# Kernel optimization log

Hardware: AMD Instinct MI355X
Metric: run time of the kernel (lower is better)

The kernel has to match this reference:

```python
import jax, jax.numpy as jnp
import numpy as np

B, SQ, QD = 8, 4096, 1280
SCTX, CD = 93, 2048
HEADS, DIM_HEAD = 20, 64
INNER = HEADS * DIM_HEAD  # 1280


def setup_inputs() -> dict:
    key = jax.random.key(0)
    ks = jax.random.split(key, 10)
    inp = {
        'x': jax.random.normal(ks[0], (B, SQ, QD), dtype=jnp.float32),
        'context': jax.random.normal(ks[1], (B, SCTX, CD), dtype=jnp.float32),
        'scale': jax.random.uniform(ks[2], (), dtype=jnp.float32),
        'num_img_token': 16,
        # learned parameters (PyTorch nn.Linear weight layout: [out, in])
        'Wq': jax.random.normal(ks[3], (INNER, QD), dtype=jnp.float32) * 0.02,
        'Wk': jax.random.normal(ks[4], (INNER, CD), dtype=jnp.float32) * 0.02,
        'Wv': jax.random.normal(ks[5], (INNER, CD), dtype=jnp.float32) * 0.02,
        'Wk_ip': jax.random.normal(ks[6], (INNER, CD), dtype=jnp.float32) * 0.02,
        'Wv_ip': jax.random.normal(ks[7], (INNER, CD), dtype=jnp.float32) * 0.02,
        'Wout': jax.random.normal(ks[8], (QD, INNER), dtype=jnp.float32) * 0.02,
        'b_out': jax.random.normal(ks[9], (QD,), dtype=jnp.float32) * 0.02,
    }
    return inp


def _heads(t):
    # [b, s, inner] -> [b, h, s, d]
    b, s, _ = t.shape
    return t.reshape(b, s, HEADS, DIM_HEAD).transpose(0, 2, 1, 3)


def _attn(q, k, v):
    # q: [b,h,sq,d], k/v: [b,h,skv,d]
    sm_scale = 1.0 / jnp.sqrt(jnp.asarray(DIM_HEAD, q.dtype))
    logits = jnp.einsum('bhqd,bhkd->bhqk', q, k) * sm_scale
    probs = jax.nn.softmax(logits, axis=-1)
    return jnp.einsum('bhqk,bhkd->bhqd', probs, v)


def reference(x, context, scale, num_img_token, Wq, Wk, Wv, Wk_ip, Wv_ip, Wout, b_out):
    eos = context.shape[1] - num_img_token
    txt_ctx = context[:, :eos, :]
    img_ctx = context[:, eos:, :]

    q = _heads(jnp.einsum('bsc,ic->bsi', x, Wq))
    k = _heads(jnp.einsum('bsc,ic->bsi', txt_ctx, Wk))
    v = _heads(jnp.einsum('bsc,ic->bsi', txt_ctx, Wv))
    k_i = _heads(jnp.einsum('bsc,ic->bsi', img_ctx, Wk_ip))
    v_i = _heads(jnp.einsum('bsc,ic->bsi', img_ctx, Wv_ip))

    txt_out = _attn(q, k, v)            # [b,h,sq,d]
    img_out = _attn(q, k_i, v_i)        # [b,h,sq,d]
    out = txt_out + scale * img_out

    out = out.transpose(0, 2, 1, 3).reshape(x.shape[0], x.shape[1], INNER)
    return jnp.einsum('bsi,oi->bso', out, Wout) + b_out
```

## Files before the change

kernel.cpp:

```cpp
#include <hip/hip_runtime.h>
#include <stdint.h>
#include <stddef.h>

typedef __attribute__((ext_vector_type(8))) short bf16x8;
typedef __attribute__((ext_vector_type(4))) short bf16x4;
typedef __attribute__((ext_vector_type(4))) float f32x4;

typedef const __attribute__((address_space(1))) uint32_t gas_u32;
typedef __attribute__((address_space(3))) uint32_t las_u32;

__device__ __forceinline__ short f2bf(float f) {
  union { float f; uint32_t u; } c; c.f = f;
  uint32_t u = c.u;
  u += 0x7fffu + ((u >> 16) & 1u);
  return (short)(u >> 16);
}

__global__ void k_cvt(const float* __restrict__ src, short* __restrict__ dst, int n) {
  int i = (blockIdx.x * 256 + threadIdx.x) * 4;
  if (i + 4 <= n) {
    float4 v = *(const float4*)(src + i);
    bf16x4 o = { f2bf(v.x), f2bf(v.y), f2bf(v.z), f2bf(v.w) };
    *(bf16x4*)(dst + i) = o;
  } else {
    for (; i < n; ++i) dst[i] = f2bf(src[i]);
  }
}

__global__ void k_cvt_ctx(const float* __restrict__ ctx, short* __restrict__ dst,
                          int rpb, int row0) {
  long total = 8L * rpb * 2048;
  long i = ((long)blockIdx.x * 256 + threadIdx.x) * 4;
  if (i >= total) return;
  int c = (int)(i & 2047);
  long rs = i >> 11;
  int b = (int)(rs / rpb);
  int s = (int)(rs - (long)b * rpb);
  const float* sp = ctx + ((long)(b * 93 + row0 + s) * 2048 + c);
  float4 v = *(const float4*)sp;
  bf16x4 o = { f2bf(v.x), f2bf(v.y), f2bf(v.z), f2bf(v.w) };
  *(bf16x4*)(dst + i) = o;
}

template <int MODE>
__global__ __launch_bounds__(256)
void k_gemm(const short* __restrict__ A, const short* __restrict__ Bm,
            void* __restrict__ out, const float* __restrict__ bias,
            int Mreal, int N, int K, int SPB) {
  __shared__ __align__(16) short As[128 * 32];
  __shared__ __align__(16) short Bs[128 * 32];
  const int t = threadIdx.x;
  const int lane = t & 63, wave = t >> 6;
  const int wm = (wave >> 1) * 64, wn = (wave & 1) * 64;
  const int m0 = blockIdx.y * 128, n0 = blockIdx.x * 128;
  const int q4 = lane >> 4, r16 = lane & 15;

  f32x4 zero = {0.f, 0.f, 0.f, 0.f};
  f32x4 acc[4][4];
#pragma unroll
  for (int i = 0; i < 4; ++i)
#pragma unroll
    for (int j = 0; j < 4; ++j) acc[i][j] = zero;

  const int p0 = t, p1 = t + 256;
  const int ar0 = p0 >> 2, ac0 = (((p0 & 3) ^ ((ar0 >> 1) & 3))) * 8;
  const int ar1 = p1 >> 2, ac1 = (((p1 & 3) ^ ((ar1 >> 1) & 3))) * 8;
  int gm0 = m0 + ar0; if (gm0 >= Mreal) gm0 = Mreal - 1;
  int gm1 = m0 + ar1; if (gm1 >= Mreal) gm1 = Mreal - 1;
  const short* ga0 = A + (size_t)gm0 * K + ac0;
  const short* ga1 = A + (size_t)gm1 * K + ac1;
  const short* gb0 = Bm + (size_t)(n0 + ar0) * K + ac0;
  const short* gb1 = Bm + (size_t)(n0 + ar1) * K + ac1;

  const int swz = (q4 ^ ((r16 >> 1) & 3)) * 8;

  for (int k0 = 0; k0 < K; k0 += 32) {
    __builtin_amdgcn_global_load_lds((gas_u32*)(ga0 + k0), (las_u32*)(As + p0 * 8), 16, 0, 0);
    __builtin_amdgcn_global_load_lds((gas_u32*)(ga1 + k0), (las_u32*)(As + p1 * 8), 16, 0, 0);
    __builtin_amdgcn_global_load_lds((gas_u32*)(gb0 + k0), (las_u32*)(Bs + p0 * 8), 16, 0, 0);
    __builtin_amdgcn_global_load_lds((gas_u32*)(gb1 + k0), (las_u32*)(Bs + p1 * 8), 16, 0, 0);
    __syncthreads();

    bf16x8 af[4], bf[4];
#pragma unroll
    for (int i = 0; i < 4; ++i)
      af[i] = *(const bf16x8*)(As + (wm + i * 16 + r16) * 32 + swz);
#pragma unroll
    for (int j = 0; j < 4; ++j)
      bf[j] = *(const bf16x8*)(Bs + (wn + j * 16 + r16) * 32 + swz);
#pragma unroll
    for (int i = 0; i < 4; ++i)
#pragma unroll
      for (int j = 0; j < 4; ++j)
        acc[i][j] = __builtin_amdgcn_mfma_f32_16x16x32_bf16(af[i], bf[j], acc[i][j], 0, 0, 0);
    __syncthreads();
  }

  if (MODE == 0) {
    short* O = (short*)out;
#pragma unroll
    for (int i = 0; i < 4; ++i) {
#pragma unroll
      for (int rr = 0; rr < 4; ++rr) {
        int m = m0 + wm + i * 16 + q4 * 4 + rr;
        if (m < Mreal) {
          int bb, ss;
          if (SPB == 4096) { bb = m >> 12; ss = m & 4095; }
          else             { bb = m / SPB; ss = m - bb * SPB; }
#pragma unroll
          for (int j = 0; j < 4; ++j) {
            int n = n0 + wn + j * 16 + r16;
            int h = n >> 6, d = n & 63;
            int grp = (h >= 20) ? 1 : 0;
            int hl = h - grp * 20;
            O[(((size_t)(grp * 160 + bb * 20 + hl)) * SPB + ss) * 64 + d] = f2bf(acc[i][j][rr]);
          }
        }
      }
    }
  } else {
    float* O = (float*)out;
#pragma unroll
    for (int i = 0; i < 4; ++i) {
#pragma unroll
      for (int rr = 0; rr < 4; ++rr) {
        int m = m0 + wm + i * 16 + q4 * 4 + rr;
        if (m < Mreal) {
#pragma unroll
          for (int j = 0; j < 4; ++j) {
            int n = n0 + wn + j * 16 + r16;
            O[(size_t)m * N + n] = acc[i][j][rr] + bias[n];
          }
        }
      }
    }
  }
}

__global__ __launch_bounds__(256)
void k_attn(const short* __restrict__ qb, const short* __restrict__ kb,
            const short* __restrict__ vb, const short* __restrict__ kib,
            const short* __restrict__ vib, const float* __restrict__ scale_p,
            short* __restrict__ out) {
  constexpr int KS = 72;
  constexpr int PS = 104;
  __shared__ __align__(16) short Ks[96 * KS];
  __shared__ __align__(16) short Vt[64 * PS];
  __shared__ __align__(16) short Pp[4][16 * PS];
  const int t = threadIdx.x, lane = t & 63, wave = t >> 6;
  const int q4 = lane >> 4, r16 = lane & 15;
  const int b = blockIdx.z, h = blockIdx.y, qt = blockIdx.x;
  const int bh = b * 20 + h;
  const short* kt = kb + (size_t)bh * 77 * 64;
  const short* vt = vb + (size_t)bh * 77 * 64;
  const short* ki = kib + (size_t)bh * 16 * 64;
  const short* vi = vib + (size_t)bh * 16 * 64;

  for (int c = t; c < 96 * 8; c += 256) {
    int row = c >> 3, o = (c & 7) * 8;
    uint4 val = {0u, 0u, 0u, 0u};
    if (row < 77)       val = *(const uint4*)(kt + row * 64 + o);
    else if (row >= 80) val = *(const uint4*)(ki + (row - 80) * 64 + o);
    *(uint4*)(Ks + row * KS + o) = val;
  }
  for (int i = t; i < 96 * 64; i += 256) {
    int key = i >> 6, d = i & 63;
    short v = 0;
    if (key < 77)       v = vt[key * 64 + d];
    else if (key >= 80) v = vi[(key - 80) * 64 + d];
    Vt[d * PS + key] = v;
  }
  __syncthreads();

  const int s0 = qt * 64 + wave * 16;
  const short* qp = qb + ((size_t)bh * 4096 + s0) * 64;
  bf16x8 qf[2];
#pragma unroll
  for (int kc = 0; kc < 2; ++kc)
    qf[kc] = *(const bf16x8*)(qp + r16 * 64 + kc * 32 + q4 * 8);

  f32x4 zero = {0.f, 0.f, 0.f, 0.f};
  f32x4 lg[6];
#pragma unroll
  for (int nt = 0; nt < 6; ++nt) {
    lg[nt] = zero;
#pragma unroll
    for (int kc = 0; kc < 2; ++kc) {
      bf16x8 kf = *(const bf16x8*)(Ks + (nt * 16 + r16) * KS + kc * 32 + q4 * 8);
      lg[nt] = __builtin_amdgcn_mfma_f32_16x16x32_bf16(qf[kc], kf, lg[nt], 0, 0, 0);
    }
  }

  const float sm = 0.125f;
  const float scl = scale_p[0];
#pragma unroll
  for (int nt = 0; nt < 6; ++nt)
#pragma unroll
    for (int rr = 0; rr < 4; ++rr) lg[nt][rr] *= sm;
  if (r16 >= 13) {
#pragma unroll
    for (int rr = 0; rr < 4; ++rr) lg[4][rr] = -1e30f;
  }

#pragma unroll
  for (int rr = 0; rr < 4; ++rr) {
    float mx = -1e30f;
#pragma unroll
    for (int nt = 0; nt < 5; ++nt) mx = fmaxf(mx, lg[nt][rr]);
#pragma unroll
    for (int o = 1; o < 16; o <<= 1) mx = fmaxf(mx, __shfl_xor(mx, o, 64));
    float s = 0.f;
#pragma unroll
    for (int nt = 0; nt < 5; ++nt) {
      float p = __expf(lg[nt][rr] - mx);
      lg[nt][rr] = p; s += p;
    }
#pragma unroll
    for (int o = 1; o < 16; o <<= 1) s += __shfl_xor(s, o, 64);
    float inv = 1.f / s;
#pragma unroll
    for (int nt = 0; nt < 5; ++nt) lg[nt][rr] *= inv;

    float mi = lg[5][rr];
#pragma unroll
    for (int o = 1; o < 16; o <<= 1) mi = fmaxf(mi, __shfl_xor(mi, o, 64));
    float pi = __expf(lg[5][rr] - mi);
    float si = pi;
#pragma unroll
    for (int o = 1; o < 16; o <<= 1) si += __shfl_xor(si, o, 64);
    lg[5][rr] = pi * (scl / si);
  }

  short* pw = &Pp[wave][0];
#pragma unroll
  for (int nt = 0; nt < 6; ++nt)
#pragma unroll
    for (int rr = 0; rr < 4; ++rr)
      pw[(q4 * 4 + rr) * PS + nt * 16 + r16] = f2bf(lg[nt][rr]);

  f32x4 oc[4];
#pragma unroll
  for (int dt = 0; dt < 4; ++dt) {
    oc[dt] = zero;
#pragma unroll
    for (int kc = 0; kc < 3; ++kc) {
      bf16x8 pf = *(const bf16x8*)(pw + r16 * PS + kc * 32 + q4 * 8);
      bf16x8 vf = *(const bf16x8*)(Vt + (dt * 16 + r16) * PS + kc * 32 + q4 * 8);
      oc[dt] = __builtin_amdgcn_mfma_f32_16x16x32_bf16(pf, vf, oc[dt], 0, 0, 0);
    }
  }

#pragma unroll
  for (int dt = 0; dt < 4; ++dt)
#pragma unroll
    for (int rr = 0; rr < 4; ++rr) {
      int m = s0 + q4 * 4 + rr;
      int d = dt * 16 + r16;
      out[((size_t)b * 4096 + m) * 1280 + h * 64 + d] = f2bf(oc[dt][rr]);
    }
}

extern "C" void kernel_launch(void* const* d_in, const int* in_sizes, int n_in,
                              void* d_out, int out_size, void* d_ws, size_t ws_size,
                              hipStream_t stream) {
  const float* x    = (const float*)d_in[0];
  const float* ctx  = (const float*)d_in[1];
  const float* scal = (const float*)d_in[2];
  const float* Wq   = (const float*)d_in[4];
  const float* Wk   = (const float*)d_in[5];
  const float* Wv   = (const float*)d_in[6];
  const float* Wkip = (const float*)d_in[7];
  const float* Wvip = (const float*)d_in[8];
  const float* Wout = (const float*)d_in[9];
  const float* bout = (const float*)d_in[10];
  float* out = (float*)d_out;

  char* ws = (char*)d_ws;
  size_t off = 0;
  auto alloc = [&](size_t elems) -> short* {
    short* p = (short*)(ws + off);
    off += (elems * 2 + 255) & ~(size_t)255;
    return p;
  };
  short* xb    = alloc(32768UL * 1280);
  short* txtb  = alloc(616UL * 2048);
  short* imgb  = alloc(128UL * 2048);
  short* Wqb   = alloc(1280UL * 1280);
  short* Wkvb  = alloc(2UL * 1280 * 2048);
  short* Wkvip = alloc(2UL * 1280 * 2048);
  short* Woutb = alloc(1280UL * 1280);
  short* qb    = alloc(32768UL * 1280);
  short* kb    = alloc(2UL * 160 * 77 * 64);
  short* kib   = alloc(2UL * 160 * 16 * 64);
  short* vb    = kb  + 160UL * 77 * 64;
  short* vib   = kib + 160UL * 16 * 64;
  short* attnb = xb;

  auto cvt = [&](const float* s, short* d, long n) {
    int blocks = (int)((n / 4 + 255) / 256);
    k_cvt<<<blocks, 256, 0, stream>>>(s, d, (int)n);
  };
  cvt(x, xb, 32768L * 1280);
  cvt(Wq, Wqb, 1280L * 1280);
  cvt(Wk,   Wkvb,                 1280L * 2048);
  cvt(Wv,   Wkvb + 1280L * 2048,  1280L * 2048);
  cvt(Wkip, Wkvip,                1280L * 2048);
  cvt(Wvip, Wkvip + 1280L * 2048, 1280L * 2048);
  cvt(Wout, Woutb, 1280L * 1280);
  {
    long n1 = 8L * 77 * 2048;
    k_cvt_ctx<<<(int)((n1 / 4 + 255) / 256), 256, 0, stream>>>(ctx, txtb, 77, 0);
    long n2 = 8L * 16 * 2048;
    k_cvt_ctx<<<(int)((n2 / 4 + 255) / 256), 256, 0, stream>>>(ctx, imgb, 16, 77);
  }

  { dim3 g(10, 256); k_gemm<0><<<g, 256, 0, stream>>>(xb, Wqb, qb, nullptr, 32768, 1280, 1280, 4096); }
  { dim3 g(20, 5);
    k_gemm<0><<<g, 256, 0, stream>>>(txtb, Wkvb, kb, nullptr, 616, 2560, 2048, 77); }
  { dim3 g(20, 1);
    k_gemm<0><<<g, 256, 0, stream>>>(imgb, Wkvip, kib, nullptr, 128, 2560, 2048, 16); }
  { dim3 g(64, 20, 8);
    k_attn<<<g, 256, 0, stream>>>(qb, kb, vb, kib, vib, scal, attnb); }
  { dim3 g(10, 256);
    k_gemm<1><<<g, 256, 0, stream>>>(attnb, Woutb, out, bout, 32768, 1280, 1280, 1); }
}
```

Baseline: 884.0 us.

## Use 256x256 multi-stage pipelined GEMM, batch conversions and KV projections

Replaces the 128x128 single-buffered GEMM with a 256x256-tile, 512-thread kernel. It keeps four LDS stages with explicit vmcnt waits so global loads overlap MFMA work, raises MFMA priority with setprio, and remaps workgroups in XCD-aware order. The seven fp32-to-bf16 conversion launches are merged into one multi-segment kernel, and the text and image K/V projections share a single launch. The cost is 128KB of LDS per block and more registers per thread, which may reduce occupancy; the small K/V GEMMs also waste more work in padded tiles.

```diff
diff --git a/kernel.cpp b/kernel.cpp
--- a/kernel.cpp
+++ b/kernel.cpp
@@ -16,15 +16,21 @@
   return (short)(u >> 16);
 }
 
-__global__ void k_cvt(const float* __restrict__ src, short* __restrict__ dst, int n) {
-  int i = (blockIdx.x * 256 + threadIdx.x) * 4;
-  if (i + 4 <= n) {
-    float4 v = *(const float4*)(src + i);
-    bf16x4 o = { f2bf(v.x), f2bf(v.y), f2bf(v.z), f2bf(v.w) };
-    *(bf16x4*)(dst + i) = o;
-  } else {
-    for (; i < n; ++i) dst[i] = f2bf(src[i]);
-  }
+struct CvtArgs {
+  const float* s[7];
+  short* d[7];
+  long cum[8];
+};
+
+__global__ void k_cvt_multi(CvtArgs a) {
+  long i = ((long)blockIdx.x * 256 + threadIdx.x) * 4;
+  if (i >= a.cum[7]) return;
+  int g = 0;
+  while (i >= a.cum[g + 1]) ++g;
+  long o = i - a.cum[g];
+  float4 v = *(const float4*)(a.s[g] + o);
+  bf16x4 ov = { f2bf(v.x), f2bf(v.y), f2bf(v.z), f2bf(v.w) };
+  *(bf16x4*)(a.d[g] + o) = ov;
 }
 
 __global__ void k_cvt_ctx(const float* __restrict__ ctx, short* __restrict__ dst,
@@ -43,89 +49,132 @@
 }
 
 template <int MODE>
-__global__ __launch_bounds__(256)
-void k_gemm(const short* __restrict__ A, const short* __restrict__ Bm,
-            void* __restrict__ out, const float* __restrict__ bias,
-            int Mreal, int N, int K, int SPB) {
-  __shared__ __align__(16) short As[128 * 32];
-  __shared__ __align__(16) short Bs[128 * 32];
+__global__ __launch_bounds__(512, 2)
+void k_gemm256(const short* __restrict__ A, const short* __restrict__ Bm,
+               void* __restrict__ out, const float* __restrict__ bias,
+               int Mreal, int N, int K, int SPB,
+               const short* __restrict__ A2, const short* __restrict__ B2,
+               void* __restrict__ out2, int Mreal2, int SPB2, int split_by) {
+  __shared__ __align__(16) short As[4][256 * 32];
+  __shared__ __align__(16) short Bs[4][256 * 32];
   const int t = threadIdx.x;
-  const int lane = t & 63, wave = t >> 6;
-  const int wm = (wave >> 1) * 64, wn = (wave & 1) * 64;
-  const int m0 = blockIdx.y * 128, n0 = blockIdx.x * 128;
+  const int lane = t & 63;
+  const int wave = t >> 6;
   const int q4 = lane >> 4, r16 = lane & 15;
+  const int wm = (wave >> 2) * 128;
+  const int wn = (wave & 3) * 64;
+
+  const int nwg = gridDim.x * gridDim.y;
+  const int lin = blockIdx.y * gridDim.x + blockIdx.x;
+  const int cpx = nwg >> 3;
+  const int wg = (lin & 7) * cpx + (lin >> 3);
+  const int bx = wg % gridDim.x;
+  int by = wg / gridDim.x;
+
+  const short* Ap = A; const short* Bp = Bm; void* op = out;
+  int Mr = Mreal, SP = SPB;
+  if (by >= split_by) { Ap = A2; Bp = B2; op = out2; Mr = Mreal2; SP = SPB2; by -= split_by; }
+  const int m0 = by * 256, n0 = bx * 256;
 
   f32x4 zero = {0.f, 0.f, 0.f, 0.f};
-  f32x4 acc[4][4];
-#pragma unroll
-  for (int i = 0; i < 4; ++i)
+  f32x4 acc[8][4];
+#pragma unroll
+  for (int i = 0; i < 8; ++i)
 #pragma unroll
     for (int j = 0; j < 4; ++j) acc[i][j] = zero;
 
-  const int p0 = t, p1 = t + 256;
-  const int ar0 = p0 >> 2, ac0 = (((p0 & 3) ^ ((ar0 >> 1) & 3))) * 8;
-  const int ar1 = p1 >> 2, ac1 = (((p1 & 3) ^ ((ar1 >> 1) & 3))) * 8;
-  int gm0 = m0 + ar0; if (gm0 >= Mreal) gm0 = Mreal - 1;
-  int gm1 = m0 + ar1; if (gm1 >= Mreal) gm1 = Mreal - 1;
-  const short* ga0 = A + (size_t)gm0 * K + ac0;
-  const short* ga1 = A + (size_t)gm1 * K + ac1;
-  const short* gb0 = Bm + (size_t)(n0 + ar0) * K + ac0;
-  const short* gb1 = Bm + (size_t)(n0 + ar1) * K + ac1;
+  const int srow = t >> 2;
+  const int csrc = (t & 3) ^ ((srow >> 1) & 3);
+  int ra0 = m0 + srow;        if (ra0 >= Mr) ra0 = Mr - 1;
+  int ra1 = m0 + 128 + srow;  if (ra1 >= Mr) ra1 = Mr - 1;
+  const short* gA0 = Ap + (size_t)ra0 * K + csrc * 8;
+  const short* gA1 = Ap + (size_t)ra1 * K + csrc * 8;
+  const short* gB0 = Bp + (size_t)(n0 + srow) * K + csrc * 8;
+  const short* gB1 = Bp + (size_t)(n0 + 128 + srow) * K + csrc * 8;
 
   const int swz = (q4 ^ ((r16 >> 1) & 3)) * 8;
 
-  for (int k0 = 0; k0 < K; k0 += 32) {
-    __builtin_amdgcn_global_load_lds((gas_u32*)(ga0 + k0), (las_u32*)(As + p0 * 8), 16, 0, 0);
-    __builtin_amdgcn_global_load_lds((gas_u32*)(ga1 + k0), (las_u32*)(As + p1 * 8), 16, 0, 0);
-    __builtin_amdgcn_global_load_lds((gas_u32*)(gb0 + k0), (las_u32*)(Bs + p0 * 8), 16, 0, 0);
-    __builtin_amdgcn_global_load_lds((gas_u32*)(gb1 + k0), (las_u32*)(Bs + p1 * 8), 16, 0, 0);
-    __syncthreads();
-
-    bf16x8 af[4], bf[4];
-#pragma unroll
-    for (int i = 0; i < 4; ++i)
-      af[i] = *(const bf16x8*)(As + (wm + i * 16 + r16) * 32 + swz);
+  auto stage = [&](int sb, int k0) {
+    short* as = &As[0][0] + sb * (256 * 32);
+    short* bs = &Bs[0][0] + sb * (256 * 32);
+    __builtin_amdgcn_global_load_lds((gas_u32*)(gA0 + k0), (las_u32*)(as + t * 8), 16, 0, 0);
+    __builtin_amdgcn_global_load_lds((gas_u32*)(gA1 + k0), (las_u32*)(as + (t + 512) * 8), 16, 0, 0);
+    __builtin_amdgcn_global_load_lds((gas_u32*)(gB0 + k0), (las_u32*)(bs + t * 8), 16, 0, 0);
+    __builtin_amdgcn_global_load_lds((gas_u32*)(gB1 + k0), (las_u32*)(bs + (t + 512) * 8), 16, 0, 0);
+  };
+
+  auto dostep = [&](int sb) {
+    const short* as = &As[0][0] + sb * (256 * 32);
+    const short* bs = &Bs[0][0] + sb * (256 * 32);
+    bf16x8 av[8], bv[4];
+#pragma unroll
+    for (int i = 0; i < 8; ++i)
+      av[i] = *(const bf16x8*)(as + (wm + i * 16 + r16) * 32 + swz);
 #pragma unroll
     for (int j = 0; j < 4; ++j)
-      bf[j] = *(const bf16x8*)(Bs + (wn + j * 16 + r16) * 32 + swz);
-#pragma unroll
-    for (int i = 0; i < 4; ++i)
+      bv[j] = *(const bf16x8*)(bs + (wn + j * 16 + r16) * 32 + swz);
+    __builtin_amdgcn_s_setprio(1);
+#pragma unroll
+    for (int i = 0; i < 8; ++i)
 #pragma unroll
       for (int j = 0; j < 4; ++j)
-        acc[i][j] = __builtin_amdgcn_mfma_f32_16x16x32_bf16(af[i], bf[j], acc[i][j], 0, 0, 0);
-    __syncthreads();
-  }
+        acc[i][j] = __builtin_amdgcn_mfma_f32_16x16x32_bf16(av[i], bv[j], acc[i][j], 0, 0, 0);
+    __builtin_amdgcn_s_setprio(0);
+    __builtin_amdgcn_s_barrier();
+  };
+
+  const int NS = K >> 5;
+
+  stage(0, 0);
+  stage(1, 32);
+  stage(2, 64);
+
+  for (int s = 0; s < NS - 3; ++s) {
+    stage((s + 3) & 3, (s + 3) * 32);
+    asm volatile("s_waitcnt vmcnt(12)" ::: "memory");
+    __builtin_amdgcn_s_barrier();
+    dostep(s & 3);
+  }
+  asm volatile("s_waitcnt vmcnt(8)" ::: "memory");
+  __builtin_amdgcn_s_barrier();
+  dostep((NS - 3) & 3);
+  asm volatile("s_waitcnt vmcnt(4)" ::: "memory");
+  __builtin_amdgcn_s_barrier();
+  dostep((NS - 2) & 3);
+  asm volatile("s_waitcnt vmcnt(0)" ::: "memory");
+  __builtin_amdgcn_s_barrier();
+  dostep((NS - 1) & 3);
 
   if (MODE == 0) {
-    short* O = (short*)out;
-#pragma unroll
-    for (int i = 0; i < 4; ++i) {
+    short* O = (short*)op;
+#pragma unroll
+    for (int i = 0; i < 8; ++i) {
 #pragma unroll
       for (int rr = 0; rr < 4; ++rr) {
         int m = m0 + wm + i * 16 + q4 * 4 + rr;
-        if (m < Mreal) {
+        if (m < Mr) {
           int bb, ss;
-          if (SPB == 4096) { bb = m >> 12; ss = m & 4095; }
-          else             { bb = m / SPB; ss = m - bb * SPB; }
+          if (SP == 4096) { bb = m >> 12; ss = m & 4095; }
+          else            { bb = m / SP; ss = m - bb * SP; }
 #pragma unroll
           for (int j = 0; j < 4; ++j) {
             int n = n0 + wn + j * 16 + r16;
             int h = n >> 6, d = n & 63;
             int grp = (h >= 20) ? 1 : 0;
             int hl = h - grp * 20;
-            O[(((size_t)(grp * 160 + bb * 20 + hl)) * SPB + ss) * 64 + d] = f2bf(acc[i][j][rr]);
+            O[(((size_t)(grp * 160 + bb * 20 + hl)) * SP + ss) * 64 + d] = f2bf(acc[i][j][rr]);
           }
         }
       }
     }
   } else {
-    float* O = (float*)out;
-#pragma unroll
-    for (int i = 0; i < 4; ++i) {
+    float* O = (float*)op;
+#pragma unroll
+    for (int i = 0; i < 8; ++i) {
 #pragma unroll
       for (int rr = 0; rr < 4; ++rr) {
         int m = m0 + wm + i * 16 + q4 * 4 + rr;
-        if (m < Mreal) {
+        if (m < Mr) {
 #pragma unroll
           for (int j = 0; j < 4; ++j) {
             int n = n0 + wn + j * 16 + r16;
@@ -296,17 +345,19 @@
   short* vib   = kib + 160UL * 16 * 64;
   short* attnb = xb;
 
-  auto cvt = [&](const float* s, short* d, long n) {
-    int blocks = (int)((n / 4 + 255) / 256);
-    k_cvt<<<blocks, 256, 0, stream>>>(s, d, (int)n);
-  };
-  cvt(x, xb, 32768L * 1280);
-  cvt(Wq, Wqb, 1280L * 1280);
-  cvt(Wk,   Wkvb,                 1280L * 2048);
-  cvt(Wv,   Wkvb + 1280L * 2048,  1280L * 2048);
-  cvt(Wkip, Wkvip,                1280L * 2048);
-  cvt(Wvip, Wkvip + 1280L * 2048, 1280L * 2048);
-  cvt(Wout, Woutb, 1280L * 1280);
+  {
+    CvtArgs a;
+    const float* srcs[7] = { x, Wq, Wk, Wv, Wkip, Wvip, Wout };
+    short* dsts[7] = { xb, Wqb, Wkvb, Wkvb + 1280L * 2048, Wkvip,
+                       Wkvip + 1280L * 2048, Woutb };
+    long ns[7] = { 32768L * 1280, 1280L * 1280, 1280L * 2048, 1280L * 2048,
+                   1280L * 2048, 1280L * 2048, 1280L * 1280 };
+    long c = 0;
+    for (int k = 0; k < 7; ++k) { a.s[k] = srcs[k]; a.d[k] = dsts[k]; a.cum[k] = c; c += ns[k]; }
+    a.cum[7] = c;
+    int blocks = (int)((c / 4 + 255) / 256);
+    k_cvt_multi<<<blocks, 256, 0, stream>>>(a);
+  }
   {
     long n1 = 8L * 77 * 2048;
     k_cvt_ctx<<<(int)((n1 / 4 + 255) / 256), 256, 0, stream>>>(ctx, txtb, 77, 0);
@@ -314,13 +365,15 @@
     k_cvt_ctx<<<(int)((n2 / 4 + 255) / 256), 256, 0, stream>>>(ctx, imgb, 16, 77);
   }
 
-  { dim3 g(10, 256); k_gemm<0><<<g, 256, 0, stream>>>(xb, Wqb, qb, nullptr, 32768, 1280, 1280, 4096); }
-  { dim3 g(20, 5);
-    k_gemm<0><<<g, 256, 0, stream>>>(txtb, Wkvb, kb, nullptr, 616, 2560, 2048, 77); }
-  { dim3 g(20, 1);
-    k_gemm<0><<<g, 256, 0, stream>>>(imgb, Wkvip, kib, nullptr, 128, 2560, 2048, 16); }
+  { dim3 g(5, 128);
+    k_gemm256<0><<<g, 512, 0, stream>>>(xb, Wqb, qb, nullptr, 32768, 1280, 1280, 4096,
+                                        nullptr, nullptr, nullptr, 0, 0, 1 << 20); }
+  { dim3 g(10, 4);
+    k_gemm256<0><<<g, 512, 0, stream>>>(txtb, Wkvb, kb, nullptr, 616, 2560, 2048, 77,
+                                        imgb, Wkvip, kib, 128, 16, 3); }
   { dim3 g(64, 20, 8);
     k_attn<<<g, 256, 0, stream>>>(qb, kb, vb, kib, vib, scal, attnb); }
-  { dim3 g(10, 256);
-    k_gemm<1><<<g, 256, 0, stream>>>(attnb, Woutb, out, bout, 32768, 1280, 1280, 1); }
-}
+  { dim3 g(5, 128);
+    k_gemm256<1><<<g, 512, 0, stream>>>(attnb, Woutb, out, bout, 32768, 1280, 1280, 1,
+                                        nullptr, nullptr, nullptr, 0, 0, 1 << 20); }
+}
```

Measured after the change: 864.0 us. 2.3% less time.
